# Performance work log

Hardware: AMD Instinct MI355X
Metric: run time of the kernel (lower is better)

Reference implementation:

```python
import jax, jax.numpy as jnp
import numpy as np

NB, BS, NHID, NINP = 6, 200, 1200, 2400  # num_blocks, block_size, nhid, ninp (=2*nhid)
T, B, NTOK = 32, 32, 16000


def _ln(x, g, b):
    mu = x.mean(-1, keepdims=True)
    v = ((x - mu) ** 2).mean(-1, keepdims=True)
    return (x - mu) / jnp.sqrt(v + 1e-5) * g + b


def _attend(q3, k3, v3, wq, wk, wv, wfc, g, b, nh, dk, dv, residual):
    # q3/k3/v3: (B, L, d_model); multi-head scaled-dot attention across blocks
    Bz, L, _ = q3.shape
    qh = (q3 @ wq).reshape(Bz, L, nh, dk)
    kh = (k3 @ wk).reshape(Bz, L, nh, dk)
    vh = (v3 @ wv).reshape(Bz, L, nh, dv)
    att = jnp.einsum('bqhd,bkhd->bhqk', qh, kh) / float(np.sqrt(dk))
    att = jax.nn.softmax(att, axis=-1)
    out = jnp.einsum('bhqk,bkhd->bqhd', att, vh).reshape(Bz, L, nh * dv)
    out = out @ wfc
    if residual:
        out = out + q3
    return _ln(out, g, b)


def setup_inputs() -> dict:
    key = jax.random.key(0)
    ks = jax.random.split(key, 16)
    rn = lambda i, sh, s: jax.random.normal(ks[i], sh, dtype=jnp.float32) * s
    d = {}
    d['tokens'] = jax.random.randint(ks[0], (T, B), 0, NTOK)
    d['h0'] = jnp.zeros((2, B, NHID), jnp.float32)
    d['c0'] = jnp.zeros((2, B, NHID), jnp.float32)
    d['emb_table'] = jax.random.uniform(ks[1], (NTOK, NINP), jnp.float32, -0.1, 0.1)
    d['Wi'] = rn(2, (NB, 4 * BS, NINP), 0.01)
    d['Wh'] = rn(3, (NB, 4 * BS, BS), 0.05)
    d['bih'] = jnp.zeros((NB, 4 * BS), jnp.float32)
    d['bhh'] = jnp.zeros((NB, 4 * BS), jnp.float32)
    d['mq'] = rn(4, (BS, 64), 0.07)
    d['mk'] = rn(5, (BS, 64), 0.07)
    d['mv'] = rn(6, (BS, 64), 0.07)
    d['mfc'] = rn(7, (64, BS), 0.1)
    d['mg'] = jnp.ones((BS,), jnp.float32)
    d['mb'] = jnp.zeros((BS,), jnp.float32)
    d['lq'] = rn(8, (BS, 1600), 0.07)
    d['lk'] = rn(9, (BS, 1600), 0.07)
    d['lv'] = rn(10, (BS, 1600), 0.07)
    d['lfc'] = rn(11, (1600, 2400), 0.02)
    d['lg'] = jnp.ones((2400,), jnp.float32)
    d['lb'] = jnp.zeros((2400,), jnp.float32)
    d['dec_w'] = jax.random.uniform(ks[12], (NTOK, NHID), jnp.float32, -0.1, 0.1)
    d['dec_b'] = jnp.zeros((NTOK,), jnp.float32)
    return d


def reference(tokens, h0, c0, emb_table, Wi, Wh, bih, bhh, mq, mk, mv, mfc, mg, mb,
              lq, lk, lv, lfc, lg, lb, dec_w, dec_b):
    def block_lstm(x, h, c):
        # block-diagonal LSTMCell: k independent cells, per-block input NINP, hidden BS
        Bz = x.shape[0]
        xb = x.reshape(Bz, NB, -1)
        hb = h.reshape(Bz, NB, BS)
        cb = c.reshape(Bz, NB, BS)
        gt = jnp.einsum('bki,kgi->bkg', xb, Wi) + jnp.einsum('bkh,kgh->bkg', hb, Wh) + bih + bhh
        ii, ff, gg, oo = jnp.split(gt, 4, axis=-1)  # torch LSTMCell gate order i,f,g,o
        cn = jax.nn.sigmoid(ff) * cb + jax.nn.sigmoid(ii) * jnp.tanh(gg)
        hn = jax.nn.sigmoid(oo) * jnp.tanh(cn)
        return hn.reshape(Bz, NHID), cn.reshape(Bz, NHID)

    def self_att(h):
        hb = h.reshape(-1, NB, BS)
        hb = _attend(hb, hb, hb, mq, mk, mv, mfc, mg, mb, 4, 16, 16, True)
        return hb.reshape(-1, NHID)

    emb = emb_table[tokens]  # (T, B, NINP)

    def step0(carry, x):
        h, c = carry
        h, c = block_lstm(jnp.tile(x, (1, NB)), h, c)
        h = self_att(h)
        return (h, c), h

    (hf0, cf0), out = jax.lax.scan(step0, (h0[0], c0[0]), emb)

    def step1(carry, x):
        h, c = carry
        q = h.reshape(-1, NB, BS)
        kv = x.reshape(-1, NB, BS)
        inp = _attend(q, kv, kv, lq, lk, lv, lfc, lg, lb, 8, BS, BS, False)  # (B, NB, 2400)
        h, c = block_lstm(inp.reshape(inp.shape[0], -1), h, c)
        h = self_att(h)
        return (h, c), h

    (hf1, cf1), out = jax.lax.scan(step1, (h0[1], c0[1]), out)

    decoded = out @ dec_w.T + dec_b  # (T, B, NTOK)
    return decoded, jnp.stack([hf0, hf1]), jnp.stack([cf0, cf1])
```

## Files before the change

kernel.cpp:

```cpp
#include <hip/hip_runtime.h>
#include <math.h>

#define NBLK 6
#define BS   200
#define NHID 1200
#define NINP 2400
#define TT   32
#define BZ   32
#define NTOK 16000
#define NG   4800
#define ROWS 1024
#define L1D  1600
#define ST   (BZ*NHID)

__device__ __forceinline__ float sigmoidf_(float x) { return 1.0f / (1.0f + expf(-x)); }

template <bool BT>
__global__ __launch_bounds__(256) void gemm128_kernel(
    const float* __restrict__ A, const float* __restrict__ B,
    const float* __restrict__ bias1, const float* __restrict__ bias2,
    float* __restrict__ C, int M, int N, int K, const int* __restrict__ a_idx)
{
    __shared__ __align__(16) float As[8][132];
    __shared__ __align__(16) float Bs[8][132];
    const int tid = threadIdx.x;
    const int tx = tid & 15, ty = tid >> 4;
    const int n0 = blockIdx.x * 128, m0 = blockIdx.y * 128;

    const int la_r = tid >> 1, la_k = (tid & 1) * 4;
    long arow;
    {
        int row = m0 + la_r;
        arow = a_idx ? (long)a_idx[row] * K : (long)row * K;
    }
    float acc[8][8] = {};

    for (int k0 = 0; k0 < K; k0 += 8) {
        {
            float4 v = *(const float4*)&A[arow + k0 + la_k];
            As[la_k + 0][la_r] = v.x;
            As[la_k + 1][la_r] = v.y;
            As[la_k + 2][la_r] = v.z;
            As[la_k + 3][la_r] = v.w;
        }
        if constexpr (!BT) {
            int kk = tid >> 5, n = (tid & 31) * 4;
            int col = n0 + n;
            float4 v = make_float4(0.f, 0.f, 0.f, 0.f);
            if (col < N) v = *(const float4*)&B[(long)(k0 + kk) * N + col];
            *(float4*)&Bs[kk][n] = v;
        } else {
            int n = tid >> 1, kk0 = (tid & 1) * 4;
            int col = n0 + n;
            float4 v = make_float4(0.f, 0.f, 0.f, 0.f);
            if (col < N) v = *(const float4*)&B[(long)col * K + k0 + kk0];
            Bs[kk0 + 0][n] = v.x;
            Bs[kk0 + 1][n] = v.y;
            Bs[kk0 + 2][n] = v.z;
            Bs[kk0 + 3][n] = v.w;
        }
        __syncthreads();
        #pragma unroll
        for (int kk = 0; kk < 8; kk++) {
            float av[8], bv[8];
            *(float4*)&av[0] = *(const float4*)&As[kk][ty * 4];
            *(float4*)&av[4] = *(const float4*)&As[kk][ty * 4 + 64];
            *(float4*)&bv[0] = *(const float4*)&Bs[kk][tx * 4];
            *(float4*)&bv[4] = *(const float4*)&Bs[kk][tx * 4 + 64];
            #pragma unroll
            for (int i = 0; i < 8; i++)
                #pragma unroll
                for (int j = 0; j < 8; j++) acc[i][j] += av[i] * bv[j];
        }
        __syncthreads();
    }
    #pragma unroll
    for (int i = 0; i < 8; i++) {
        int row = m0 + ty * 4 + (i & 3) + (i >> 2) * 64;
        #pragma unroll
        for (int jg = 0; jg < 2; jg++) {
            int col = n0 + tx * 4 + jg * 64;
            if (col < N) {
                float4 v;
                v.x = acc[i][jg * 4 + 0]; v.y = acc[i][jg * 4 + 1];
                v.z = acc[i][jg * 4 + 2]; v.w = acc[i][jg * 4 + 3];
                if (bias1) {
                    float4 b1 = *(const float4*)&bias1[col];
                    v.x += b1.x; v.y += b1.y; v.z += b1.z; v.w += b1.w;
                }
                if (bias2) {
                    float4 b2 = *(const float4*)&bias2[col];
                    v.x += b2.x; v.y += b2.y; v.z += b2.z; v.w += b2.w;
                }
                *(float4*)&C[(long)row * N + col] = v;
            }
        }
    }
}

__global__ __launch_bounds__(256) void bigb_kernel(
    const float* __restrict__ lq, const float* __restrict__ lk,
    float* __restrict__ BigB)
{
    int id = blockIdx.x * 256 + threadIdx.x;
    if (id >= 320000) return;
    int h = id / 40000, r = id % 40000, cp = r / 200, c = r % 200;
    const float4* a = (const float4*)(lq + (long)c * L1D + h * 200);
    const float4* b = (const float4*)(lk + (long)cp * L1D + h * 200);
    float s0 = 0, s1 = 0, s2 = 0, s3 = 0;
    #pragma unroll 5
    for (int d = 0; d < 50; d++) {
        float4 av = a[d], bv = b[d];
        s0 += av.x * bv.x; s1 += av.y * bv.y; s2 += av.z * bv.z; s3 += av.w * bv.w;
    }
    BigB[(long)cp * L1D + h * 200 + c] = s0 + s1 + s2 + s3;
}

__global__ __launch_bounds__(256) void whT_kernel(
    const float* __restrict__ Wh, float* __restrict__ WhT)
{
    int id = blockIdx.x * 256 + threadIdx.x;
    if (id >= 960000) return;
    int k = id / 160000, r = id % 160000, m = r / 800, g = r % 800;
    WhT[id] = Wh[(long)(k * 800 + g) * 200 + m];
}

template <int NT>
__device__ __forceinline__ void att_inline(
    float* hb, float* aux, float* gout,
    const float* __restrict__ mq, const float* __restrict__ mk,
    const float* __restrict__ mv, const float* __restrict__ mfc,
    const float* __restrict__ mg, const float* __restrict__ mb)
{
    const int tid = threadIdx.x;
    float* qh   = aux;
    float* kh   = aux + 384;
    float* vh   = aux + 768;
    float* att  = aux + 1152;
    float* outp = aux + 1296;
    float* o2   = aux + 1680;
    float* mu_s = aux + 2880;
    float* rs_s = aux + 2888;
    if (tid < 192) {
        int which = tid >> 6, hd = tid & 63;
        const float* Mw = which == 0 ? mq : (which == 1 ? mk : mv);
        float acc[6] = {};
        for (int jx = 0; jx < 200; jx++) {
            float w = Mw[jx * 64 + hd];
            #pragma unroll
            for (int l = 0; l < 6; l++) acc[l] += hb[l * 200 + jx] * w;
        }
        float* dst = which == 0 ? qh : (which == 1 ? kh : vh);
        #pragma unroll
        for (int l = 0; l < 6; l++) dst[l * 64 + hd] = acc[l];
    }
    __syncthreads();
    if (tid < 144) {
        int h = tid / 36, r = tid % 36, q = r / 6, kk = r % 6;
        float s = 0;
        #pragma unroll
        for (int d = 0; d < 16; d++) s += qh[q * 64 + h * 16 + d] * kh[kk * 64 + h * 16 + d];
        att[(h * 6 + q) * 6 + kk] = s * 0.25f;
    }
    __syncthreads();
    if (tid < 24) {
        float* a = att + tid * 6;
        float mx = a[0];
        for (int i = 1; i < 6; i++) mx = fmaxf(mx, a[i]);
        float sm = 0;
        for (int i = 0; i < 6; i++) { a[i] = expf(a[i] - mx); sm += a[i]; }
        float inv = 1.f / sm;
        for (int i = 0; i < 6; i++) a[i] *= inv;
    }
    __syncthreads();
    for (int id = tid; id < 384; id += NT) {
        int q = id >> 6, hd = id & 63, h = hd >> 4;
        float s = 0;
        #pragma unroll
        for (int kk = 0; kk < 6; kk++) s += att[(h * 6 + q) * 6 + kk] * vh[kk * 64 + hd];
        outp[id] = s;
    }
    __syncthreads();
    if (tid < 200) {
        float acc[6] = {};
        for (int d = 0; d < 64; d++) {
            float w = mfc[d * 200 + tid];
            #pragma unroll
            for (int q = 0; q < 6; q++) acc[q] += outp[q * 64 + d] * w;
        }
        #pragma unroll
        for (int q = 0; q < 6; q++) o2[q * 200 + tid] = acc[q] + hb[q * 200 + tid];
    }
    __syncthreads();
    if (tid < 6) {
        const float4* o4 = (const float4*)(o2 + tid * 200);
        float s = 0, s2 = 0;
        for (int i = 0; i < 50; i++) {
            float4 v = o4[i];
            s += v.x + v.y + v.z + v.w;
            s2 += v.x * v.x + v.y * v.y + v.z * v.z + v.w * v.w;
        }
        float mu = s / 200.f;
        float var = s2 / 200.f - mu * mu;
        mu_s[tid] = mu;
        rs_s[tid] = 1.0f / sqrtf(var + 1e-5f);
    }
    __syncthreads();
    for (int i = tid; i < 300; i += NT) {
        int q = i / 50;
        float4 v = ((float4*)o2)[i];
        float4 g4 = ((const float4*)mg)[i % 50];
        float4 b4 = ((const float4*)mb)[i % 50];
        float mu = mu_s[q], rstd = rs_s[q];
        float4 r;
        r.x = (v.x - mu) * rstd * g4.x + b4.x;
        r.y = (v.y - mu) * rstd * g4.y + b4.y;
        r.z = (v.z - mu) * rstd * g4.z + b4.z;
        r.w = (v.w - mu) * rstd * g4.w + b4.w;
        ((float4*)hb)[i] = r;
        if (gout) ((float4*)(gout))[i] = r;
    }
    __syncthreads();
}

__global__ __launch_bounds__(1024) void phaseA_kernel(
    const float* __restrict__ GX0, const float* __restrict__ h0,
    const float* __restrict__ c0, const float* __restrict__ WhT,
    float* __restrict__ out0, float* __restrict__ cf0,
    const float* __restrict__ mq, const float* __restrict__ mk,
    const float* __restrict__ mv, const float* __restrict__ mfc,
    const float* __restrict__ mg, const float* __restrict__ mb)
{
    __shared__ __align__(16) float h_s[1200];
    __shared__ __align__(16) float c_s[1200];
    __shared__ __align__(16) float g_s[4800];
    __shared__ __align__(16) float ps[4800];
    const int b = blockIdx.x, tid = threadIdx.x;
    for (int i = tid; i < 300; i += 1024) {
        ((float4*)h_s)[i] = ((const float4*)(h0 + b * NHID))[i];
        ((float4*)c_s)[i] = ((const float4*)(c0 + b * NHID))[i];
    }
    __syncthreads();
    for (int t = 0; t < TT; t++) {
        for (int tau = tid; tau < 2400; tau += 1024) {
            int mh = (tau >= 1200);
            int slot = tau - mh * 1200;
            int k = slot / 200, g4 = slot - k * 200;
            const float* wp = WhT + (long)k * 160000 + (long)mh * 80000 + g4 * 4;
            const float* hp2 = h_s + k * 200 + mh * 100;
            float a0 = 0, a1 = 0, a2 = 0, a3 = 0;
            #pragma unroll 4
            for (int m = 0; m < 100; m++) {
                float hv = hp2[m];
                float4 w = *(const float4*)(wp + (long)m * 800);
                a0 += hv * w.x; a1 += hv * w.y; a2 += hv * w.z; a3 += hv * w.w;
            }
            float* dst = mh ? ps : g_s;
            int o = k * 800 + g4 * 4;
            dst[o] = a0; dst[o + 1] = a1; dst[o + 2] = a2; dst[o + 3] = a3;
        }
        __syncthreads();
        const float* gxp = GX0 + ((long)t * BZ + b) * NG;
        for (int idx = tid; idx < 1200; idx += 1024) {
            int k = idx / 200, j = idx - k * 200;
            int base = k * 800 + j;
            float gi = g_s[base]       + ps[base]       + gxp[base];
            float gf = g_s[base + 200] + ps[base + 200] + gxp[base + 200];
            float gg = g_s[base + 400] + ps[base + 400] + gxp[base + 400];
            float go = g_s[base + 600] + ps[base + 600] + gxp[base + 600];
            float cn = sigmoidf_(gf) * c_s[idx] + sigmoidf_(gi) * tanhf(gg);
            c_s[idx] = cn;
            h_s[idx] = sigmoidf_(go) * tanhf(cn);
        }
        __syncthreads();
        att_inline<1024>(h_s, ps, out0 + (long)t * ST + b * NHID, mq, mk, mv, mfc, mg, mb);
    }
    for (int i = tid; i < 300; i += 1024)
        ((float4*)(cf0 + b * NHID))[i] = ((float4*)c_s)[i];
}

template <bool FIRST>
__global__ __launch_bounds__(256) void fusedatt_kernel(
    const float* __restrict__ htmp, const float* __restrict__ h0l1,
    float* __restrict__ out1_prev,
    const float* __restrict__ KMt, const float* __restrict__ VHt,
    const float* __restrict__ lfc, float* __restrict__ Fp,
    const float* __restrict__ mq, const float* __restrict__ mk,
    const float* __restrict__ mv, const float* __restrict__ mfc,
    const float* __restrict__ mg, const float* __restrict__ mb)
{
    __shared__ __align__(16) float hb[1200];
    __shared__ __align__(16) float aux[2896];
    __shared__ __align__(16) float a_s[1200];
    __shared__ float attp[72];
    __shared__ float attr[36];
    const int blk = blockIdx.x, b = blk >> 3, h = blk & 7, tid = threadIdx.x;
    if (FIRST) {
        for (int i = tid; i < 300; i += 256)
            ((float4*)hb)[i] = ((const float4*)(h0l1 + b * NHID))[i];
        __syncthreads();
    } else {
        for (int i = tid; i < 300; i += 256)
            ((float4*)hb)[i] = ((const float4*)(htmp + b * NHID))[i];
        __syncthreads();
        att_inline<256>(hb, aux, (h == 0) ? out1_prev + b * NHID : nullptr,
                        mq, mk, mv, mfc, mg, mb);
    }
    const float* kb = KMt + (long)b * 9600 + h * 200;
    if (tid < 72) {
        int r = tid >> 1, half = tid & 1;
        int q = r / 6, kk = r % 6;
        const float4* qr = (const float4*)(hb + q * 200 + half * 100);
        const float4* kr = (const float4*)(kb + (long)kk * L1D + half * 100);
        float s0 = 0, s1 = 0, s2 = 0, s3 = 0;
        #pragma unroll 5
        for (int d = 0; d < 25; d++) {
            float4 a = qr[d], v = kr[d];
            s0 += a.x * v.x; s1 += a.y * v.y; s2 += a.z * v.z; s3 += a.w * v.w;
        }
        attp[tid] = s0 + s1 + s2 + s3;
    }
    __syncthreads();
    if (tid < 6) {
        float v[6]; float mx = -1e30f;
        #pragma unroll
        for (int kk = 0; kk < 6; kk++) {
            float s = (attp[(tid * 6 + kk) * 2] + attp[(tid * 6 + kk) * 2 + 1]) * 0.07071067811865475f;
            v[kk] = s; mx = fmaxf(mx, s);
        }
        float sm = 0;
        #pragma unroll
        for (int kk = 0; kk < 6; kk++) { v[kk] = expf(v[kk] - mx); sm += v[kk]; }
        float inv = 1.f / sm;
        #pragma unroll
        for (int kk = 0; kk < 6; kk++) attr[tid * 6 + kk] = v[kk] * inv;
    }
    __syncthreads();
    if (tid < 200) {
        int hd = h * 200 + tid;
        const float* vb = VHt + (long)b * 9600 + hd;
        float v0 = vb[0], v1 = vb[L1D], v2 = vb[2 * L1D];
        float v3 = vb[3 * L1D], v4 = vb[4 * L1D], v5 = vb[5 * L1D];
        #pragma unroll
        for (int q = 0; q < 6; q++) {
            const float* a = attr + q * 6;
            a_s[q * 200 + tid] =
                a[0] * v0 + a[1] * v1 + a[2] * v2 + a[3] * v3 + a[4] * v4 + a[5] * v5;
        }
    }
    __syncthreads();
    const float4* lfc4 = (const float4*)lfc;
    for (int c4 = tid; c4 < 600; c4 += 256) {
        float4 acc[6] = {};
        #pragma unroll 2
        for (int m = 0; m < 200; m++) {
            float4 w = lfc4[(long)(h * 200 + m) * 600 + c4];
            #pragma unroll
            for (int q = 0; q < 6; q++) {
                float a = a_s[q * 200 + m];
                acc[q].x += a * w.x; acc[q].y += a * w.y;
                acc[q].z += a * w.z; acc[q].w += a * w.w;
            }
        }
        #pragma unroll
        for (int q = 0; q < 6; q++)
            *(float4*)&Fp[((long)h * 192 + b * 6 + q) * NINP + c4 * 4] = acc[q];
    }
}

__global__ __launch_bounds__(256) void attsmall_kernel(
    const float* __restrict__ h_in, float* __restrict__ h_out,
    const float* __restrict__ mq, const float* __restrict__ mk,
    const float* __restrict__ mv, const float* __restrict__ mfc,
    const float* __restrict__ mg, const float* __restrict__ mb)
{
    __shared__ __align__(16) float hb[1200];
    __shared__ __align__(16) float aux[2896];
    const int b = blockIdx.x, tid = threadIdx.x;
    for (int i = tid; i < 300; i += 256)
        ((float4*)hb)[i] = ((const float4*)(h_in + b * NHID))[i];
    __syncthreads();
    att_inline<256>(hb, aux, h_out + b * NHID, mq, mk, mv, mfc, mg, mb);
}

__global__ __launch_bounds__(256) void ln_sum8_kernel(
    const float* __restrict__ Fp, float* __restrict__ Y,
    const float* __restrict__ g, const float* __restrict__ bta)
{
    __shared__ float rowbuf[2400];
    __shared__ float aw[4], bw[4];
    const int r = blockIdx.x, tid = threadIdx.x;
    const long SL = (long)192 * NINP / 4;
    const float4* f0 = (const float4*)(Fp) + (long)r * (NINP / 4);
    float s = 0, s2 = 0;
    for (int i = tid; i < 600; i += 256) {
        float4 v = f0[i];
        #pragma unroll
        for (int z = 1; z < 8; z++) {
            float4 a = f0[(long)z * SL + i];
            v.x += a.x; v.y += a.y; v.z += a.z; v.w += a.w;
        }
        ((float4*)rowbuf)[i] = v;
        s += v.x + v.y + v.z + v.w;
        s2 += v.x * v.x + v.y * v.y + v.z * v.z + v.w * v.w;
    }
    for (int off = 32; off; off >>= 1) { s += __shfl_down(s, off); s2 += __shfl_down(s2, off); }
    int wid = tid >> 6, lane = tid & 63;
    if (lane == 0) { aw[wid] = s; bw[wid] = s2; }
    __syncthreads();
    if (tid == 0) {
        float a = 0, a2 = 0;
        for (int w = 0; w < 4; w++) { a += aw[w]; a2 += bw[w]; }
        float mu = a / NINP;
        float var = a2 / NINP - mu * mu;
        aw[0] = mu;
        bw[0] = 1.0f / sqrtf(var + 1e-5f);
    }
    __syncthreads();
    float mu = aw[0], rstd = bw[0];
    for (int i = tid; i < 600; i += 256) {
        float4 v = ((float4*)rowbuf)[i];
        float4 g4 = ((const float4*)g)[i];
        float4 b4 = ((const float4*)bta)[i];
        float4 o;
        o.x = (v.x - mu) * rstd * g4.x + b4.x;
        o.y = (v.y - mu) * rstd * g4.y + b4.y;
        o.z = (v.z - mu) * rstd * g4.z + b4.z;
        o.w = (v.w - mu) * rstd * g4.w + b4.w;
        ((float4*)(Y + (long)r * NINP))[i] = o;
    }
}

__global__ __launch_bounds__(512) void lstm1_kernel(
    const float* __restrict__ inp, const float* __restrict__ hprev,
    float* __restrict__ c_io, const float* __restrict__ Wi,
    const float* __restrict__ Wh, const float* __restrict__ bih,
    const float* __restrict__ bhh, float* __restrict__ h_out)
{
    __shared__ float h_s[200 * 33];
    __shared__ float x_s[2][100 * 33];
    __shared__ float ps[12][128];
    const int k = blockIdx.y, jt = blockIdx.x, tid = threadIdx.x;
    const int b = tid & 31, jg = (tid >> 5) & 3, kh = tid >> 7;
    const int j = jt * 4 + jg;

    for (int idx = tid; idx < 1600; idx += 512) {
        int bb = idx / 50, m4 = idx % 50;
        float4 v = *(const float4*)&hprev[bb * NHID + k * BS + m4 * 4];
        h_s[(m4 * 4 + 0) * 33 + bb] = v.x;
        h_s[(m4 * 4 + 1) * 33 + bb] = v.y;
        h_s[(m4 * 4 + 2) * 33 + bb] = v.z;
        h_s[(m4 * 4 + 3) * 33 + bb] = v.w;
    }
    for (int idx = tid; idx < 800; idx += 512) {
        int bb = idx / 25, m4 = idx % 25;
        float4 v = *(const float4*)&inp[(long)(bb * 6 + k) * NINP + m4 * 4];
        x_s[0][(m4 * 4 + 0) * 33 + bb] = v.x;
        x_s[0][(m4 * 4 + 1) * 33 + bb] = v.y;
        x_s[0][(m4 * 4 + 2) * 33 + bb] = v.z;
        x_s[0][(m4 * 4 + 3) * 33 + bb] = v.w;
    }

    const float* wi0 = Wi + (long)(k * 800 + j) * NINP;
    const float* wi1 = wi0 + (long)200 * NINP;
    const float* wi2 = wi0 + (long)400 * NINP;
    const float* wi3 = wi0 + (long)600 * NINP;
    float a0 = 0, a1 = 0, a2 = 0, a3 = 0;
    int cur = 0;
    for (int ti = 0; ti < 24; ti++) {
        __syncthreads();
        if (ti + 1 < 24) {
            int kt = (ti + 1) * 100;
            float* xs = x_s[cur ^ 1];
            for (int idx = tid; idx < 800; idx += 512) {
                int bb = idx / 25, m4 = idx % 25;
                float4 v = *(const float4*)&inp[(long)(bb * 6 + k) * NINP + kt + m4 * 4];
                xs[(m4 * 4 + 0) * 33 + bb] = v.x;
                xs[(m4 * 4 + 1) * 33 + bb] = v.y;
                xs[(m4 * 4 + 2) * 33 + bb] = v.z;
                xs[(m4 * 4 + 3) * 33 + bb] = v.w;
            }
        }
        if (ti / 6 == kh) {
            const int kt = ti * 100;
            const float* xs = x_s[cur];
            for (int m = 0; m < 100; m += 4) {
                float4 w0 = *(const float4*)&wi0[kt + m];
                float4 w1 = *(const float4*)&wi1[kt + m];
                float4 w2 = *(const float4*)&wi2[kt + m];
                float4 w3 = *(const float4*)&wi3[kt + m];
                float x0 = xs[(m + 0) * 33 + b], x1 = xs[(m + 1) * 33 + b];
                float x2 = xs[(m + 2) * 33 + b], x3 = xs[(m + 3) * 33 + b];
                a0 += x0 * w0.x + x1 * w0.y + x2 * w0.z + x3 * w0.w;
                a1 += x0 * w1.x + x1 * w1.y + x2 * w1.z + x3 * w1.w;
                a2 += x0 * w2.x + x1 * w2.y + x2 * w2.z + x3 * w2.w;
                a3 += x0 * w3.x + x1 * w3.y + x2 * w3.z + x3 * w3.w;
            }
        }
        cur ^= 1;
    }
    if (kh == 0) {
        const float* w0 = Wh + (long)(k * 800 + j) * 200;
        const float* w1 = w0 + 200 * 200;
        const float* w2 = w0 + 400 * 200;
        const float* w3 = w0 + 600 * 200;
        for (int m = 0; m < 200; m += 4) {
            float4 wv0 = *(const float4*)&w0[m];
            float4 wv1 = *(const float4*)&w1[m];
            float4 wv2 = *(const float4*)&w2[m];
            float4 wv3 = *(const float4*)&w3[m];
            float h0v = h_s[(m + 0) * 33 + b], h1v = h_s[(m + 1) * 33 + b];
            float h2v = h_s[(m + 2) * 33 + b], h3v = h_s[(m + 3) * 33 + b];
            a0 += h0v * wv0.x + h1v * wv0.y + h2v * wv0.z + h3v * wv0.w;
            a1 += h0v * wv1.x + h1v * wv1.y + h2v * wv1.z + h3v * wv1.w;
            a2 += h0v * wv2.x + h1v * wv2.y + h2v * wv2.z + h3v * wv2.w;
            a3 += h0v * wv3.x + h1v * wv3.y + h2v * wv3.z + h3v * wv3.w;
        }
    } else {
        int g = (kh - 1) * 4, t2 = tid & 127;
        ps[g + 0][t2] = a0; ps[g + 1][t2] = a1; ps[g + 2][t2] = a2; ps[g + 3][t2] = a3;
    }
    __syncthreads();
    if (kh == 0) {
        a0 += ps[0][tid] + ps[4][tid] + ps[8][tid];
        a1 += ps[1][tid] + ps[5][tid] + ps[9][tid];
        a2 += ps[2][tid] + ps[6][tid] + ps[10][tid];
        a3 += ps[3][tid] + ps[7][tid] + ps[11][tid];
        int nb2 = k * 800;
        float gi = a0 + bih[nb2 + j] + bhh[nb2 + j];
        float gf = a1 + bih[nb2 + 200 + j] + bhh[nb2 + 200 + j];
        float gg = a2 + bih[nb2 + 400 + j] + bhh[nb2 + 400 + j];
        float go = a3 + bih[nb2 + 600 + j] + bhh[nb2 + 600 + j];
        int o = b * NHID + k * BS + j;
        float cold = c_io[o];
        float cn = sigmoidf_(gf) * cold + sigmoidf_(gi) * tanhf(gg);
        float hn = sigmoidf_(go) * tanhf(cn);
        c_io[o] = cn;
        h_out[o] = hn;
    }
}

extern "C" void kernel_launch(void* const* d_in, const int* in_sizes, int n_in,
                              void* d_out, int out_size, void* d_ws, size_t ws_size,
                              hipStream_t stream)
{
    const int*   tokens = (const int*)  d_in[0];
    const float* h0     = (const float*)d_in[1];
    const float* c0     = (const float*)d_in[2];
    const float* emb    = (const float*)d_in[3];
    const float* Wi     = (const float*)d_in[4];
    const float* Wh     = (const float*)d_in[5];
    const float* bih    = (const float*)d_in[6];
    const float* bhh    = (const float*)d_in[7];
    const float* mq     = (const float*)d_in[8];
    const float* mk     = (const float*)d_in[9];
    const float* mv     = (const float*)d_in[10];
    const float* mfc    = (const float*)d_in[11];
    const float* mg     = (const float*)d_in[12];
    const float* mb     = (const float*)d_in[13];
    const float* lq     = (const float*)d_in[14];
    const float* lk     = (const float*)d_in[15];
    const float* lv     = (const float*)d_in[16];
    const float* lfc    = (const float*)d_in[17];
    const float* lg     = (const float*)d_in[18];
    const float* lb     = (const float*)d_in[19];
    const float* dec_w  = (const float*)d_in[20];
    const float* dec_b  = (const float*)d_in[21];
    float* out = (float*)d_out;

    float* p = (float*)d_ws;
    float* GX0  = p; p += (long)ROWS * NG;
    float* out0 = p; p += (long)ROWS * NHID;
    float* out1 = p; p += (long)ROWS * NHID;
    float* KM   = p; p += (long)ROWS * 6 * L1D;
    float* VH1  = p; p += (long)ROWS * 6 * L1D;
    float* FCp  = p; p += (long)8 * 192 * NINP;
    float* inp  = p; p += 192 * NINP;
    float* htmp = p; p += BZ * NHID;
    float* cb1  = p; p += BZ * NHID;
    float* BigB = p; p += 200 * L1D;
    float* WhT  = p; p += 6 * 200 * 800;

    long off = (long)ROWS * NTOK;
    float* cf0 = out + off + 2 * ST;

    hipMemcpyAsync(cb1, c0 + ST, ST * sizeof(float), hipMemcpyDeviceToDevice, stream);

    bigb_kernel<<<1250, 256, 0, stream>>>(lq, lk, BigB);
    whT_kernel<<<3750, 256, 0, stream>>>(Wh, WhT);

    gemm128_kernel<true><<<dim3(NG / 128 + 1, ROWS / 128), 256, 0, stream>>>(
        emb, Wi, bih, bhh, GX0, ROWS, NG, NINP, tokens);

    phaseA_kernel<<<BZ, 1024, 0, stream>>>(
        GX0, h0, c0, WhT, out0, cf0, mq, mk, mv, mfc, mg, mb);

    gemm128_kernel<false><<<dim3((L1D + 127) / 128, (ROWS * 6) / 128), 256, 0, stream>>>(
        out0, BigB, nullptr, nullptr, KM, ROWS * 6, L1D, BS, nullptr);
    gemm128_kernel<false><<<dim3((L1D + 127) / 128, (ROWS * 6) / 128), 256, 0, stream>>>(
        out0, lv, nullptr, nullptr, VH1, ROWS * 6, L1D, BS, nullptr);

    for (int t = 0; t < TT; t++) {
        const float* hp = (t == 0) ? h0 + ST : out1 + (long)(t - 1) * ST;
        const float* KMt = KM + (long)t * BZ * 6 * L1D;
        const float* VHt = VH1 + (long)t * BZ * 6 * L1D;
        if (t == 0) {
            fusedatt_kernel<true><<<256, 256, 0, stream>>>(
                nullptr, h0 + ST, nullptr, KMt, VHt, lfc, FCp, mq, mk, mv, mfc, mg, mb);
        } else {
            fusedatt_kernel<false><<<256, 256, 0, stream>>>(
                htmp, nullptr, out1 + (long)(t - 1) * ST, KMt, VHt, lfc, FCp,
                mq, mk, mv, mfc, mg, mb);
        }
        ln_sum8_kernel<<<192, 256, 0, stream>>>(FCp, inp, lg, lb);
        lstm1_kernel<<<dim3(50, 6), 512, 0, stream>>>(inp, hp, cb1, Wi, Wh, bih, bhh, htmp);
    }
    attsmall_kernel<<<BZ, 256, 0, stream>>>(htmp, out1 + (long)31 * ST, mq, mk, mv, mfc, mg, mb);

    gemm128_kernel<true><<<dim3(NTOK / 128, ROWS / 128), 256, 0, stream>>>(
        out1, dec_w, dec_b, nullptr, out, ROWS, NTOK, NHID, nullptr);

    hipMemcpyAsync(out + off,          out0 + (long)31 * ST, ST * sizeof(float), hipMemcpyDeviceToDevice, stream);
    hipMemcpyAsync(out + off + ST,     out1 + (long)31 * ST, ST * sizeof(float), hipMemcpyDeviceToDevice, stream);
    hipMemcpyAsync(out + off + 3 * ST, cb1,                  ST * sizeof(float), hipMemcpyDeviceToDevice, stream);
}
```

Measured before the change: 12.56 ms.

## Prefold lv·lfc weights, piggyback next-step projections, fuse layernorm into LSTM kernel

Multiplies lv and lfc per head ahead of time, so the second-layer attention applies softmax weights straight to the pre-projected value rows instead of running a per-step lfc GEMM. The next timestep's value projections are computed by extra blocks appended to the per-step kernels, overlapping them with the recurrence. The ln_sum8 kernel is removed: partial row statistics are written out and layernorm is applied while loading inputs in the LSTM kernel. The phase-A recurrent matvec is also restructured to one task per output with five independent accumulators. This adds a large double-buffered workspace and reassociates floating-point sums.

```diff
diff --git a/kernel.cpp b/kernel.cpp
--- a/kernel.cpp
+++ b/kernel.cpp
@@ -93,6 +93,136 @@
                     v.x += b2.x; v.y += b2.y; v.z += b2.z; v.w += b2.w;
                 }
                 *(float4*)&C[(long)row * N + col] = v;
+            }
+        }
+    }
+}
+
+__global__ __launch_bounds__(256) void gemmz_kernel(
+    const float* __restrict__ A, const float* __restrict__ B, float* __restrict__ C,
+    int M, int N, int K,
+    long a_rstride, long a_zoff, long b_zoff, long c_rstride, long c_zoff)
+{
+    __shared__ __align__(16) float As[8][132];
+    __shared__ __align__(16) float Bs[8][132];
+    const int tid = threadIdx.x;
+    const int tx = tid & 15, ty = tid >> 4;
+    const int n0 = blockIdx.x * 128, m0 = blockIdx.y * 128;
+    const int z = blockIdx.z;
+    const float* Az = A + a_zoff * z;
+    const float* Bz = B + b_zoff * z;
+    float* Cz = C + c_zoff * z;
+
+    const int la_r = tid >> 1, la_k = (tid & 1) * 4;
+    int arow_i = m0 + la_r; if (arow_i >= M) arow_i = M - 1;
+    const long arow = (long)arow_i * a_rstride;
+    float acc[8][8] = {};
+
+    for (int k0 = 0; k0 < K; k0 += 8) {
+        {
+            float4 v = *(const float4*)&Az[arow + k0 + la_k];
+            As[la_k + 0][la_r] = v.x;
+            As[la_k + 1][la_r] = v.y;
+            As[la_k + 2][la_r] = v.z;
+            As[la_k + 3][la_r] = v.w;
+        }
+        {
+            int kk = tid >> 5, n = (tid & 31) * 4;
+            int col = n0 + n;
+            float4 v = make_float4(0.f, 0.f, 0.f, 0.f);
+            if (col < N) v = *(const float4*)&Bz[(long)(k0 + kk) * N + col];
+            *(float4*)&Bs[kk][n] = v;
+        }
+        __syncthreads();
+        #pragma unroll
+        for (int kk = 0; kk < 8; kk++) {
+            float av[8], bv[8];
+            *(float4*)&av[0] = *(const float4*)&As[kk][ty * 4];
+            *(float4*)&av[4] = *(const float4*)&As[kk][ty * 4 + 64];
+            *(float4*)&bv[0] = *(const float4*)&Bs[kk][tx * 4];
+            *(float4*)&bv[4] = *(const float4*)&Bs[kk][tx * 4 + 64];
+            #pragma unroll
+            for (int i = 0; i < 8; i++)
+                #pragma unroll
+                for (int j = 0; j < 8; j++) acc[i][j] += av[i] * bv[j];
+        }
+        __syncthreads();
+    }
+    #pragma unroll
+    for (int i = 0; i < 8; i++) {
+        int row = m0 + ty * 4 + (i & 3) + (i >> 2) * 64;
+        if (row >= M) continue;
+        #pragma unroll
+        for (int jg = 0; jg < 2; jg++) {
+            int col = n0 + tx * 4 + jg * 64;
+            if (col < N) {
+                float4 v;
+                v.x = acc[i][jg * 4 + 0]; v.y = acc[i][jg * 4 + 1];
+                v.z = acc[i][jg * 4 + 2]; v.w = acc[i][jg * 4 + 3];
+                *(float4*)&Cz[(long)row * c_rstride + col] = v;
+            }
+        }
+    }
+}
+
+__device__ __forceinline__ void piggy_tile(
+    float* smem, int tid, bool act,
+    const float* __restrict__ A,
+    const float* __restrict__ B,
+    float* __restrict__ C,
+    int mt, int nt)
+{
+    float* As = smem;
+    float* Bs = smem + 1056;
+    const int tx = tid & 15, ty = (tid >> 4) & 15;
+    const int n0 = nt * 128, m0 = mt * 128;
+    const int la_r = (tid & 255) >> 1, la_k = (tid & 1) * 4;
+    int arow_i = m0 + la_r; if (arow_i > 191) arow_i = 191;
+    float acc[8][8] = {};
+    for (int k0 = 0; k0 < 200; k0 += 8) {
+        if (act) {
+            float4 v = *(const float4*)&A[(long)arow_i * 200 + k0 + la_k];
+            As[(la_k + 0) * 132 + la_r] = v.x;
+            As[(la_k + 1) * 132 + la_r] = v.y;
+            As[(la_k + 2) * 132 + la_r] = v.z;
+            As[(la_k + 3) * 132 + la_r] = v.w;
+            int kk = (tid >> 5) & 7, n = (tid & 31) * 4;
+            int col = n0 + n;
+            float4 w = make_float4(0.f, 0.f, 0.f, 0.f);
+            if (col < NINP) w = *(const float4*)&B[(long)(k0 + kk) * NINP + col];
+            *(float4*)&Bs[kk * 132 + n] = w;
+        }
+        __syncthreads();
+        if (act) {
+            #pragma unroll
+            for (int kk = 0; kk < 8; kk++) {
+                float av[8], bv[8];
+                *(float4*)&av[0] = *(const float4*)&As[kk * 132 + ty * 4];
+                *(float4*)&av[4] = *(const float4*)&As[kk * 132 + ty * 4 + 64];
+                *(float4*)&bv[0] = *(const float4*)&Bs[kk * 132 + tx * 4];
+                *(float4*)&bv[4] = *(const float4*)&Bs[kk * 132 + tx * 4 + 64];
+                #pragma unroll
+                for (int i = 0; i < 8; i++)
+                    #pragma unroll
+                    for (int j = 0; j < 8; j++) acc[i][j] += av[i] * bv[j];
+            }
+        }
+        __syncthreads();
+    }
+    if (act) {
+        #pragma unroll
+        for (int i = 0; i < 8; i++) {
+            int row = m0 + ty * 4 + (i & 3) + (i >> 2) * 64;
+            if (row >= 192) continue;
+            #pragma unroll
+            for (int jg = 0; jg < 2; jg++) {
+                int col = n0 + tx * 4 + jg * 64;
+                if (col < NINP) {
+                    float4 v;
+                    v.x = acc[i][jg * 4 + 0]; v.y = acc[i][jg * 4 + 1];
+                    v.z = acc[i][jg * 4 + 2]; v.w = acc[i][jg * 4 + 3];
+                    *(float4*)&C[(long)row * (8L * NINP) + col] = v;
+                }
             }
         }
     }
@@ -234,7 +364,7 @@
     __shared__ __align__(16) float h_s[1200];
     __shared__ __align__(16) float c_s[1200];
     __shared__ __align__(16) float g_s[4800];
-    __shared__ __align__(16) float ps[4800];
+    __shared__ __align__(16) float aux_s[2896];
     const int b = blockIdx.x, tid = threadIdx.x;
     for (int i = tid; i < 300; i += 1024) {
         ((float4*)h_s)[i] = ((const float4*)(h0 + b * NHID))[i];
@@ -242,207 +372,201 @@
     }
     __syncthreads();
     for (int t = 0; t < TT; t++) {
-        for (int tau = tid; tau < 2400; tau += 1024) {
-            int mh = (tau >= 1200);
-            int slot = tau - mh * 1200;
-            int k = slot / 200, g4 = slot - k * 200;
-            const float* wp = WhT + (long)k * 160000 + (long)mh * 80000 + g4 * 4;
-            const float* hp2 = h_s + k * 200 + mh * 100;
-            float a0 = 0, a1 = 0, a2 = 0, a3 = 0;
-            #pragma unroll 4
-            for (int m = 0; m < 100; m++) {
-                float hv = hp2[m];
-                float4 w = *(const float4*)(wp + (long)m * 800);
-                a0 += hv * w.x; a1 += hv * w.y; a2 += hv * w.z; a3 += hv * w.w;
+        for (int task = tid; task < 1200; task += 1024) {
+            int k = task / 200, g = task - k * 200;
+            const float* wp = WhT + (long)k * 160000 + g * 4;
+            const float* hp2 = h_s + k * 200;
+            float a0x = 0, a0y = 0, a0z = 0, a0w = 0;
+            float a1x = 0, a1y = 0, a1z = 0, a1w = 0;
+            float a2x = 0, a2y = 0, a2z = 0, a2w = 0;
+            float a3x = 0, a3y = 0, a3z = 0, a3w = 0;
+            float a4x = 0, a4y = 0, a4z = 0, a4w = 0;
+            #pragma unroll 2
+            for (int m = 0; m < 40; m++) {
+                float h0v = hp2[m], h1v = hp2[m + 40], h2v = hp2[m + 80];
+                float h3v = hp2[m + 120], h4v = hp2[m + 160];
+                float4 w0 = *(const float4*)(wp + (long)m * 800);
+                float4 w1 = *(const float4*)(wp + (long)(m + 40) * 800);
+                float4 w2 = *(const float4*)(wp + (long)(m + 80) * 800);
+                float4 w3 = *(const float4*)(wp + (long)(m + 120) * 800);
+                float4 w4 = *(const float4*)(wp + (long)(m + 160) * 800);
+                a0x += h0v * w0.x; a0y += h0v * w0.y; a0z += h0v * w0.z; a0w += h0v * w0.w;
+                a1x += h1v * w1.x; a1y += h1v * w1.y; a1z += h1v * w1.z; a1w += h1v * w1.w;
+                a2x += h2v * w2.x; a2y += h2v * w2.y; a2z += h2v * w2.z; a2w += h2v * w2.w;
+                a3x += h3v * w3.x; a3y += h3v * w3.y; a3z += h3v * w3.z; a3w += h3v * w3.w;
+                a4x += h4v * w4.x; a4y += h4v * w4.y; a4z += h4v * w4.z; a4w += h4v * w4.w;
             }
-            float* dst = mh ? ps : g_s;
-            int o = k * 800 + g4 * 4;
-            dst[o] = a0; dst[o + 1] = a1; dst[o + 2] = a2; dst[o + 3] = a3;
+            int o = k * 800 + g * 4;
+            g_s[o]     = a0x + a1x + a2x + a3x + a4x;
+            g_s[o + 1] = a0y + a1y + a2y + a3y + a4y;
+            g_s[o + 2] = a0z + a1z + a2z + a3z + a4z;
+            g_s[o + 3] = a0w + a1w + a2w + a3w + a4w;
         }
         __syncthreads();
         const float* gxp = GX0 + ((long)t * BZ + b) * NG;
         for (int idx = tid; idx < 1200; idx += 1024) {
             int k = idx / 200, j = idx - k * 200;
             int base = k * 800 + j;
-            float gi = g_s[base]       + ps[base]       + gxp[base];
-            float gf = g_s[base + 200] + ps[base + 200] + gxp[base + 200];
-            float gg = g_s[base + 400] + ps[base + 400] + gxp[base + 400];
-            float go = g_s[base + 600] + ps[base + 600] + gxp[base + 600];
+            float gi = g_s[base]       + gxp[base];
+            float gf = g_s[base + 200] + gxp[base + 200];
+            float gg = g_s[base + 400] + gxp[base + 400];
+            float go = g_s[base + 600] + gxp[base + 600];
             float cn = sigmoidf_(gf) * c_s[idx] + sigmoidf_(gi) * tanhf(gg);
             c_s[idx] = cn;
             h_s[idx] = sigmoidf_(go) * tanhf(cn);
         }
         __syncthreads();
-        att_inline<1024>(h_s, ps, out0 + (long)t * ST + b * NHID, mq, mk, mv, mfc, mg, mb);
+        att_inline<1024>(h_s, aux_s, out0 + (long)t * ST + b * NHID, mq, mk, mv, mfc, mg, mb);
     }
     for (int i = tid; i < 300; i += 1024)
         ((float4*)(cf0 + b * NHID))[i] = ((float4*)c_s)[i];
 }
 
 template <bool FIRST>
-__global__ __launch_bounds__(256) void fusedatt_kernel(
-    const float* __restrict__ htmp, const float* __restrict__ h0l1,
-    float* __restrict__ out1_prev,
-    const float* __restrict__ KMt, const float* __restrict__ VHt,
-    const float* __restrict__ lfc, float* __restrict__ Fp,
+__global__ __launch_bounds__(256) void fusedattF_kernel(
+    const float* __restrict__ hraw, float* __restrict__ out1_prev,
+    const float* __restrict__ KMt, const float* __restrict__ VFhc,
+    float* __restrict__ Fbuf, float* __restrict__ pstat,
+    const float* __restrict__ out0_next, const float* __restrict__ LVF,
+    float* __restrict__ VFh_next,
     const float* __restrict__ mq, const float* __restrict__ mk,
     const float* __restrict__ mv, const float* __restrict__ mfc,
     const float* __restrict__ mg, const float* __restrict__ mb)
 {
-    __shared__ __align__(16) float hb[1200];
-    __shared__ __align__(16) float aux[2896];
-    __shared__ __align__(16) float a_s[1200];
-    __shared__ float attp[72];
-    __shared__ float attr[36];
-    const int blk = blockIdx.x, b = blk >> 3, h = blk & 7, tid = threadIdx.x;
-    if (FIRST) {
-        for (int i = tid; i < 300; i += 256)
-            ((float4*)hb)[i] = ((const float4*)(h0l1 + b * NHID))[i];
-        __syncthreads();
-    } else {
-        for (int i = tid; i < 300; i += 256)
-            ((float4*)hb)[i] = ((const float4*)(htmp + b * NHID))[i];
-        __syncthreads();
-        att_inline<256>(hb, aux, (h == 0) ? out1_prev + b * NHID : nullptr,
+    __shared__ __align__(16) float smem[4608];
+    const int blk = blockIdx.x, tid = threadIdx.x;
+    if (blk >= 256) {
+        int pid = blk - 256;
+        int z = pid / 38, r = pid % 38, mt = r / 19, nt = r % 19;
+        piggy_tile(smem, tid, true, out0_next, LVF + (long)z * 200 * NINP,
+                   VFh_next + (long)z * NINP, mt, nt);
+        return;
+    }
+    const int b = blk >> 3, cc = blk & 7;
+    float* hb   = smem;
+    float* aux  = smem + 1200;
+    float* attp = smem + 4096;
+    float* aw   = smem + 4384;
+    float* bw   = smem + 4408;
+    for (int i = tid; i < 300; i += 256)
+        ((float4*)hb)[i] = ((const float4*)(hraw + b * NHID))[i];
+    __syncthreads();
+    if (!FIRST)
+        att_inline<256>(hb, aux, (cc == 0) ? out1_prev + b * NHID : nullptr,
                         mq, mk, mv, mfc, mg, mb);
-    }
-    const float* kb = KMt + (long)b * 9600 + h * 200;
-    if (tid < 72) {
-        int r = tid >> 1, half = tid & 1;
-        int q = r / 6, kk = r % 6;
-        const float4* qr = (const float4*)(hb + q * 200 + half * 100);
-        const float4* kr = (const float4*)(kb + (long)kk * L1D + half * 100);
+    for (int id = tid; id < 288; id += 256) {
+        int h = id / 36, r = id % 36, q = r / 6, kk = r % 6;
+        const float4* qr = (const float4*)(hb + q * 200);
+        const float4* kr = (const float4*)(KMt + (long)(b * 6 + kk) * L1D + h * 200);
         float s0 = 0, s1 = 0, s2 = 0, s3 = 0;
         #pragma unroll 5
-        for (int d = 0; d < 25; d++) {
+        for (int d = 0; d < 50; d++) {
             float4 a = qr[d], v = kr[d];
             s0 += a.x * v.x; s1 += a.y * v.y; s2 += a.z * v.z; s3 += a.w * v.w;
         }
-        attp[tid] = s0 + s1 + s2 + s3;
-    }
-    __syncthreads();
-    if (tid < 6) {
-        float v[6]; float mx = -1e30f;
-        #pragma unroll
-        for (int kk = 0; kk < 6; kk++) {
-            float s = (attp[(tid * 6 + kk) * 2] + attp[(tid * 6 + kk) * 2 + 1]) * 0.07071067811865475f;
-            v[kk] = s; mx = fmaxf(mx, s);
-        }
+        attp[(h * 6 + q) * 6 + kk] = (s0 + s1 + s2 + s3) * 0.07071067811865475f;
+    }
+    __syncthreads();
+    if (tid < 48) {
+        float* a = attp + tid * 6;
+        float mx = a[0];
+        for (int i = 1; i < 6; i++) mx = fmaxf(mx, a[i]);
         float sm = 0;
-        #pragma unroll
-        for (int kk = 0; kk < 6; kk++) { v[kk] = expf(v[kk] - mx); sm += v[kk]; }
+        for (int i = 0; i < 6; i++) { a[i] = expf(a[i] - mx); sm += a[i]; }
         float inv = 1.f / sm;
-        #pragma unroll
-        for (int kk = 0; kk < 6; kk++) attr[tid * 6 + kk] = v[kk] * inv;
-    }
-    __syncthreads();
-    if (tid < 200) {
-        int hd = h * 200 + tid;
-        const float* vb = VHt + (long)b * 9600 + hd;
-        float v0 = vb[0], v1 = vb[L1D], v2 = vb[2 * L1D];
-        float v3 = vb[3 * L1D], v4 = vb[4 * L1D], v5 = vb[5 * L1D];
-        #pragma unroll
-        for (int q = 0; q < 6; q++) {
-            const float* a = attr + q * 6;
-            a_s[q * 200 + tid] =
-                a[0] * v0 + a[1] * v1 + a[2] * v2 + a[3] * v3 + a[4] * v4 + a[5] * v5;
-        }
-    }
-    __syncthreads();
-    const float4* lfc4 = (const float4*)lfc;
-    for (int c4 = tid; c4 < 600; c4 += 256) {
-        float4 acc[6] = {};
+        for (int i = 0; i < 6; i++) a[i] *= inv;
+    }
+    __syncthreads();
+    const int cbase = cc * 300;
+    const int c0 = cbase + tid;
+    const bool has1 = tid < 44;
+    const int c1 = cbase + 256 + tid;
+    float f0[6] = {}, f1[6] = {};
+    const float* vb0 = VFhc + (long)b * 48 * NINP;
+    for (int kk = 0; kk < 6; kk++) {
         #pragma unroll 2
-        for (int m = 0; m < 200; m++) {
-            float4 w = lfc4[(long)(h * 200 + m) * 600 + c4];
+        for (int h = 0; h < 8; h++) {
+            const float* vr = vb0 + (long)(kk * 8 + h) * NINP;
+            float v0 = vr[c0];
+            float v1 = has1 ? vr[c1] : 0.f;
+            const float* pw = attp + h * 36 + kk;
             #pragma unroll
             for (int q = 0; q < 6; q++) {
-                float a = a_s[q * 200 + m];
-                acc[q].x += a * w.x; acc[q].y += a * w.y;
-                acc[q].z += a * w.z; acc[q].w += a * w.w;
+                float w = pw[q * 6];
+                f0[q] += w * v0;
+                f1[q] += w * v1;
             }
         }
-        #pragma unroll
-        for (int q = 0; q < 6; q++)
-            *(float4*)&Fp[((long)h * 192 + b * 6 + q) * NINP + c4 * 4] = acc[q];
-    }
-}
-
-__global__ __launch_bounds__(256) void attsmall_kernel(
-    const float* __restrict__ h_in, float* __restrict__ h_out,
-    const float* __restrict__ mq, const float* __restrict__ mk,
-    const float* __restrict__ mv, const float* __restrict__ mfc,
-    const float* __restrict__ mg, const float* __restrict__ mb)
-{
-    __shared__ __align__(16) float hb[1200];
-    __shared__ __align__(16) float aux[2896];
-    const int b = blockIdx.x, tid = threadIdx.x;
-    for (int i = tid; i < 300; i += 256)
-        ((float4*)hb)[i] = ((const float4*)(h_in + b * NHID))[i];
-    __syncthreads();
-    att_inline<256>(hb, aux, h_out + b * NHID, mq, mk, mv, mfc, mg, mb);
-}
-
-__global__ __launch_bounds__(256) void ln_sum8_kernel(
-    const float* __restrict__ Fp, float* __restrict__ Y,
-    const float* __restrict__ g, const float* __restrict__ bta)
-{
-    __shared__ float rowbuf[2400];
-    __shared__ float aw[4], bw[4];
-    const int r = blockIdx.x, tid = threadIdx.x;
-    const long SL = (long)192 * NINP / 4;
-    const float4* f0 = (const float4*)(Fp) + (long)r * (NINP / 4);
-    float s = 0, s2 = 0;
-    for (int i = tid; i < 600; i += 256) {
-        float4 v = f0[i];
-        #pragma unroll
-        for (int z = 1; z < 8; z++) {
-            float4 a = f0[(long)z * SL + i];
-            v.x += a.x; v.y += a.y; v.z += a.z; v.w += a.w;
-        }
-        ((float4*)rowbuf)[i] = v;
-        s += v.x + v.y + v.z + v.w;
-        s2 += v.x * v.x + v.y * v.y + v.z * v.z + v.w * v.w;
-    }
-    for (int off = 32; off; off >>= 1) { s += __shfl_down(s, off); s2 += __shfl_down(s2, off); }
+    }
+    float s[6], s2[6];
+    #pragma unroll
+    for (int q = 0; q < 6; q++) {
+        Fbuf[(long)(b * 6 + q) * NINP + c0] = f0[q];
+        if (has1) Fbuf[(long)(b * 6 + q) * NINP + c1] = f1[q];
+        s[q] = f0[q] + f1[q];
+        s2[q] = f0[q] * f0[q] + f1[q] * f1[q];
+    }
+    for (int off = 32; off; off >>= 1) {
+        #pragma unroll
+        for (int q = 0; q < 6; q++) {
+            s[q] += __shfl_down(s[q], off);
+            s2[q] += __shfl_down(s2[q], off);
+        }
+    }
     int wid = tid >> 6, lane = tid & 63;
-    if (lane == 0) { aw[wid] = s; bw[wid] = s2; }
-    __syncthreads();
-    if (tid == 0) {
-        float a = 0, a2 = 0;
-        for (int w = 0; w < 4; w++) { a += aw[w]; a2 += bw[w]; }
-        float mu = a / NINP;
-        float var = a2 / NINP - mu * mu;
-        aw[0] = mu;
-        bw[0] = 1.0f / sqrtf(var + 1e-5f);
-    }
-    __syncthreads();
-    float mu = aw[0], rstd = bw[0];
-    for (int i = tid; i < 600; i += 256) {
-        float4 v = ((float4*)rowbuf)[i];
-        float4 g4 = ((const float4*)g)[i];
-        float4 b4 = ((const float4*)bta)[i];
-        float4 o;
-        o.x = (v.x - mu) * rstd * g4.x + b4.x;
-        o.y = (v.y - mu) * rstd * g4.y + b4.y;
-        o.z = (v.z - mu) * rstd * g4.z + b4.z;
-        o.w = (v.w - mu) * rstd * g4.w + b4.w;
-        ((float4*)(Y + (long)r * NINP))[i] = o;
-    }
-}
-
-__global__ __launch_bounds__(512) void lstm1_kernel(
-    const float* __restrict__ inp, const float* __restrict__ hprev,
-    float* __restrict__ c_io, const float* __restrict__ Wi,
-    const float* __restrict__ Wh, const float* __restrict__ bih,
-    const float* __restrict__ bhh, float* __restrict__ h_out)
+    if (lane == 0) {
+        #pragma unroll
+        for (int q = 0; q < 6; q++) { aw[wid * 6 + q] = s[q]; bw[wid * 6 + q] = s2[q]; }
+    }
+    __syncthreads();
+    if (tid < 6) {
+        float S = 0, S2 = 0;
+        #pragma unroll
+        for (int w = 0; w < 4; w++) { S += aw[w * 6 + tid]; S2 += bw[w * 6 + tid]; }
+        pstat[((long)(b * 6 + tid) * 8 + cc) * 2]     = S;
+        pstat[((long)(b * 6 + tid) * 8 + cc) * 2 + 1] = S2;
+    }
+}
+
+__global__ __launch_bounds__(512) void lstm1ln_kernel(
+    const float* __restrict__ Fbuf, const float* __restrict__ pstat,
+    const float* __restrict__ lgw, const float* __restrict__ lbw,
+    const float* __restrict__ hprev, float* __restrict__ c_io,
+    const float* __restrict__ Wi, const float* __restrict__ Wh,
+    const float* __restrict__ bih, const float* __restrict__ bhh,
+    float* __restrict__ h_out,
+    const float* __restrict__ out0_next, const float* __restrict__ LVF,
+    float* __restrict__ VFh_next)
 {
     __shared__ float h_s[200 * 33];
     __shared__ float x_s[2][100 * 33];
     __shared__ float ps[12][128];
-    const int k = blockIdx.y, jt = blockIdx.x, tid = threadIdx.x;
+    __shared__ float mu_ln[32], rs_ln[32];
+    const int blk = blockIdx.x, tid = threadIdx.x;
+    if (blk >= 300) {
+        int pid = blk - 300;
+        int z = 4 + pid / 38, r = pid % 38, mt = r / 19, nt = r % 19;
+        piggy_tile(h_s, tid, tid < 256, out0_next, LVF + (long)z * 200 * NINP,
+                   VFh_next + (long)z * NINP, mt, nt);
+        return;
+    }
+    const int k = blk % 6, jt = blk / 6;
     const int b = tid & 31, jg = (tid >> 5) & 3, kh = tid >> 7;
     const int j = jt * 4 + jg;
+
+    if (tid < 32) {
+        float S = 0, S2 = 0;
+        int row = tid * 6 + k;
+        #pragma unroll
+        for (int c2 = 0; c2 < 8; c2++) {
+            S  += pstat[((long)row * 8 + c2) * 2];
+            S2 += pstat[((long)row * 8 + c2) * 2 + 1];
+        }
+        float mu = S / (float)NINP;
+        mu_ln[tid] = mu;
+        rs_ln[tid] = 1.0f / sqrtf(S2 / (float)NINP - mu * mu + 1e-5f);
+    }
+    __syncthreads();
 
     for (int idx = tid; idx < 1600; idx += 512) {
         int bb = idx / 50, m4 = idx % 50;
@@ -454,11 +578,16 @@
     }
     for (int idx = tid; idx < 800; idx += 512) {
         int bb = idx / 25, m4 = idx % 25;
-        float4 v = *(const float4*)&inp[(long)(bb * 6 + k) * NINP + m4 * 4];
-        x_s[0][(m4 * 4 + 0) * 33 + bb] = v.x;
-        x_s[0][(m4 * 4 + 1) * 33 + bb] = v.y;
-        x_s[0][(m4 * 4 + 2) * 33 + bb] = v.z;
-        x_s[0][(m4 * 4 + 3) * 33 + bb] = v.w;
+        int c = m4 * 4;
+        int row = bb * 6 + k;
+        float4 f = *(const float4*)&Fbuf[(long)row * NINP + c];
+        float4 g4 = *(const float4*)&lgw[c];
+        float4 b4 = *(const float4*)&lbw[c];
+        float mu = mu_ln[bb], rs = rs_ln[bb];
+        x_s[0][(m4 * 4 + 0) * 33 + bb] = (f.x - mu) * rs * g4.x + b4.x;
+        x_s[0][(m4 * 4 + 1) * 33 + bb] = (f.y - mu) * rs * g4.y + b4.y;
+        x_s[0][(m4 * 4 + 2) * 33 + bb] = (f.z - mu) * rs * g4.z + b4.z;
+        x_s[0][(m4 * 4 + 3) * 33 + bb] = (f.w - mu) * rs * g4.w + b4.w;
     }
 
     const float* wi0 = Wi + (long)(k * 800 + j) * NINP;
@@ -474,11 +603,16 @@
             float* xs = x_s[cur ^ 1];
             for (int idx = tid; idx < 800; idx += 512) {
                 int bb = idx / 25, m4 = idx % 25;
-                float4 v = *(const float4*)&inp[(long)(bb * 6 + k) * NINP + kt + m4 * 4];
-                xs[(m4 * 4 + 0) * 33 + bb] = v.x;
-                xs[(m4 * 4 + 1) * 33 + bb] = v.y;
-                xs[(m4 * 4 + 2) * 33 + bb] = v.z;
-                xs[(m4 * 4 + 3) * 33 + bb] = v.w;
+                int c = kt + m4 * 4;
+                int row = bb * 6 + k;
+                float4 f = *(const float4*)&Fbuf[(long)row * NINP + c];
+                float4 g4 = *(const float4*)&lgw[c];
+                float4 b4 = *(const float4*)&lbw[c];
+                float mu = mu_ln[bb], rs = rs_ln[bb];
+                xs[(m4 * 4 + 0) * 33 + bb] = (f.x - mu) * rs * g4.x + b4.x;
+                xs[(m4 * 4 + 1) * 33 + bb] = (f.y - mu) * rs * g4.y + b4.y;
+                xs[(m4 * 4 + 2) * 33 + bb] = (f.z - mu) * rs * g4.z + b4.z;
+                xs[(m4 * 4 + 3) * 33 + bb] = (f.w - mu) * rs * g4.w + b4.w;
             }
         }
         if (ti / 6 == kh) {
@@ -538,6 +672,21 @@
         c_io[o] = cn;
         h_out[o] = hn;
     }
+}
+
+__global__ __launch_bounds__(256) void attsmall_kernel(
+    const float* __restrict__ h_in, float* __restrict__ h_out,
+    const float* __restrict__ mq, const float* __restrict__ mk,
+    const float* __restrict__ mv, const float* __restrict__ mfc,
+    const float* __restrict__ mg, const float* __restrict__ mb)
+{
+    __shared__ __align__(16) float hb[1200];
+    __shared__ __align__(16) float aux[2896];
+    const int b = blockIdx.x, tid = threadIdx.x;
+    for (int i = tid; i < 300; i += 256)
+        ((float4*)hb)[i] = ((const float4*)(h_in + b * NHID))[i];
+    __syncthreads();
+    att_inline<256>(hb, aux, h_out + b * NHID, mq, mk, mv, mfc, mg, mb);
 }
 
 extern "C" void kernel_launch(void* const* d_in, const int* in_sizes, int n_in,
@@ -569,17 +718,19 @@
     float* out = (float*)d_out;
 
     float* p = (float*)d_ws;
-    float* GX0  = p; p += (long)ROWS * NG;
-    float* out0 = p; p += (long)ROWS * NHID;
-    float* out1 = p; p += (long)ROWS * NHID;
-    float* KM   = p; p += (long)ROWS * 6 * L1D;
-    float* VH1  = p; p += (long)ROWS * 6 * L1D;
-    float* FCp  = p; p += (long)8 * 192 * NINP;
-    float* inp  = p; p += 192 * NINP;
-    float* htmp = p; p += BZ * NHID;
-    float* cb1  = p; p += BZ * NHID;
-    float* BigB = p; p += 200 * L1D;
-    float* WhT  = p; p += 6 * 200 * 800;
+    float* GX0   = p; p += (long)ROWS * NG;
+    float* out0  = p; p += (long)ROWS * NHID;
+    float* out1  = p; p += (long)ROWS * NHID;
+    float* KM    = p; p += (long)ROWS * 6 * L1D;
+    float* Fbuf  = p; p += 192 * NINP;
+    float* pstat = p; p += 4096;
+    float* htmp  = p; p += BZ * NHID;
+    float* cb1   = p; p += BZ * NHID;
+    float* BigB  = p; p += 200 * L1D;
+    float* WhT   = p; p += 6 * 200 * 800;
+    float* LVF   = p; p += (long)8 * 200 * NINP;
+    float* VFhC  = p; p += (long)2 * 192 * 8 * NINP;
+    const long SLOT = (long)192 * 8 * NINP;
 
     long off = (long)ROWS * NTOK;
     float* cf0 = out + off + 2 * ST;
@@ -597,24 +748,38 @@
 
     gemm128_kernel<false><<<dim3((L1D + 127) / 128, (ROWS * 6) / 128), 256, 0, stream>>>(
         out0, BigB, nullptr, nullptr, KM, ROWS * 6, L1D, BS, nullptr);
-    gemm128_kernel<false><<<dim3((L1D + 127) / 128, (ROWS * 6) / 128), 256, 0, stream>>>(
-        out0, lv, nullptr, nullptr, VH1, ROWS * 6, L1D, BS, nullptr);
+
+    gemmz_kernel<<<dim3((NINP + 127) / 128, 2, 8), 256, 0, stream>>>(
+        lv, lfc, LVF, 200, NINP, 200,
+        (long)L1D, 200L, (long)200 * NINP, (long)NINP, (long)200 * NINP);
+
+    gemmz_kernel<<<dim3((NINP + 127) / 128, 2, 8), 256, 0, stream>>>(
+        out0, LVF, VFhC, 192, NINP, 200,
+        200L, 0L, (long)200 * NINP, (long)8 * NINP, (long)NINP);
 
     for (int t = 0; t < TT; t++) {
         const float* hp = (t == 0) ? h0 + ST : out1 + (long)(t - 1) * ST;
         const float* KMt = KM + (long)t * BZ * 6 * L1D;
-        const float* VHt = VH1 + (long)t * BZ * 6 * L1D;
+        const float* VFhc = VFhC + (long)(t & 1) * SLOT;
+        const bool hasNext = (t + 1 < TT);
+        const float* o0n = hasNext ? out0 + (long)(t + 1) * ST : nullptr;
+        float* vfn = VFhC + (long)((t + 1) & 1) * SLOT;
+        int gA = 256 + (hasNext ? 152 : 0);
+        int gL = 300 + (hasNext ? 152 : 0);
         if (t == 0) {
-            fusedatt_kernel<true><<<256, 256, 0, stream>>>(
-                nullptr, h0 + ST, nullptr, KMt, VHt, lfc, FCp, mq, mk, mv, mfc, mg, mb);
+            fusedattF_kernel<true><<<gA, 256, 0, stream>>>(
+                h0 + ST, nullptr, KMt, VFhc, Fbuf, pstat,
+                o0n, LVF, vfn, mq, mk, mv, mfc, mg, mb);
         } else {
-            fusedatt_kernel<false><<<256, 256, 0, stream>>>(
-                htmp, nullptr, out1 + (long)(t - 1) * ST, KMt, VHt, lfc, FCp,
-                mq, mk, mv, mfc, mg, mb);
-        }
-        ln_sum8_kernel<<<192, 256, 0, stream>>>(FCp, inp, lg, lb);
-        lstm1_kernel<<<dim3(50, 6), 512, 0, stream>>>(inp, hp, cb1, Wi, Wh, bih, bhh, htmp);
-    }
+            fusedattF_kernel<false><<<gA, 256, 0, stream>>>(
+                htmp, out1 + (long)(t - 1) * ST, KMt, VFhc, Fbuf, pstat,
+                o0n, LVF, vfn, mq, mk, mv, mfc, mg, mb);
+        }
+        lstm1ln_kernel<<<gL, 512, 0, stream>>>(
+            Fbuf, pstat, lg, lb, hp, cb1, Wi, Wh, bih, bhh, htmp,
+            o0n, LVF, vfn);
+    }
+
     attsmall_kernel<<<BZ, 256, 0, stream>>>(htmp, out1 + (long)31 * ST, mq, mk, mv, mfc, mg, mb);
 
     gemm128_kernel<true><<<dim3(NTOK / 128, ROWS / 128), 256, 0, stream>>>(
```

Result: faster. 10.21 ms (-18.7%).
